# Kernel tuning notes

Measured on AMD Instinct MI355X. Metric: run time of the kernel, lower is better.

The kernel has to match this reference:

```python
import jax, jax.numpy as jnp
import numpy as np

N = 50000
E = 800000
R = 8
F_IN = 128
H = 128          # num_hidden
F_OUT = 128      # num_outputs
D1, D2, D3 = 2 * H, H, F_OUT


def _glorot(key, shape):
    fan_in, fan_out = shape[-2], shape[-1]
    lim = np.sqrt(6.0 / (fan_in + fan_out)).astype(np.float32)
    return jax.random.uniform(key, shape, jnp.float32, -lim, lim)


def setup_inputs() -> dict:
    key = jax.random.key(0)
    ks = jax.random.split(key, 12)
    x = jax.random.normal(ks[0], (N, F_IN), jnp.float32)
    edge_index = jax.random.randint(ks[1], (2, E), 0, N, jnp.int64)
    edge_type = jax.random.randint(ks[2], (E,), 0, R, jnp.int64)
    return {
        "x": x,
        "edge_index": edge_index,
        "edge_type": edge_type,
        "w1": _glorot(ks[3], (R, F_IN, D1)),
        "root1": _glorot(ks[4], (F_IN, D1)),
        "b1": jnp.zeros((D1,), jnp.float32),
        "w2": _glorot(ks[5], (R, D1, D2)),
        "root2": _glorot(ks[6], (D1, D2)),
        "b2": jnp.zeros((D2,), jnp.float32),
        "w3": _glorot(ks[7], (R, D2, D3)),
        "root3": _glorot(ks[8], (D2, D3)),
        "b3": jnp.zeros((D3,), jnp.float32),
    }


def _rgcn_layer(h, src, dst, seg, inv_cnt, W, root, bias):
    # Per-relation mean aggregation via a fused (dst, rel) segment id,
    # then a grouped contraction with the per-relation weights.
    n, fin = h.shape
    s = jax.ops.segment_sum(h[src], seg, num_segments=n * R)  # [N*R, fin]
    agg = s.reshape(n, R, fin) * inv_cnt                      # mean per (node, rel)
    return jnp.einsum("nri,rio->no", agg, W) + h @ root + bias


def reference(x, edge_index, edge_type, w1, root1, b1, w2, root2, b2, w3, root3, b3):
    src, dst = edge_index[0], edge_index[1]
    seg = dst * R + edge_type                                  # fused (dst, rel) id
    cnt = jax.ops.segment_sum(jnp.ones((E,), x.dtype), seg, num_segments=N * R)
    inv_cnt = (1.0 / jnp.maximum(cnt, 1.0)).reshape(N, R, 1)

    h1 = jax.nn.elu(_rgcn_layer(x, src, dst, seg, inv_cnt, w1, root1, b1))
    # dropout: identity (eval mode)
    h2 = jax.nn.elu(_rgcn_layer(h1, src, dst, seg, inv_cnt, w2, root2, b2))
    h3 = jax.nn.elu(_rgcn_layer(h2, src, dst, seg, inv_cnt, w3, root3, b3))
    return jnp.concatenate([h1, h2, h3], axis=1)               # [N, D1+D2+D3]
```

## Files before the change

### kernel.cpp

```cpp
#include <hip/hip_runtime.h>


#define DEVI __device__ __forceinline__

constexpr int NN    = 50000;
constexpr int EE    = 800000;
constexpr int RREL  = 8;
constexpr int NRSEG = NN * RREL;

using u16 = unsigned short;
using u32 = unsigned int;
using u64 = unsigned long long;

typedef short short8 __attribute__((ext_vector_type(8)));
typedef float f32x4  __attribute__((ext_vector_type(4)));

DEVI float bf2f(u32 u){ union{u32 i; float f;} x; x.i = u << 16; return x.f; }
DEVI u16   f2b(float f){ u32 u = __float_as_uint(f); u32 r = u + 0x7fffu + ((u >> 16) & 1u); return (u16)(r >> 16); }

typedef const __attribute__((address_space(1))) u32 gas_u32;
typedef __attribute__((address_space(3))) u32       las_u32;
DEVI void gload16(const void* g, void* l){
  __builtin_amdgcn_global_load_lds((gas_u32*)(u64)g, (las_u32*)(u64)l, 16, 0, 0);
}


__global__ void count_k(const int* __restrict__ dst, const int* __restrict__ et, int* __restrict__ cnt){
  int e = blockIdx.x * 256 + threadIdx.x;
  if(e < EE) atomicAdd(&cnt[dst[e] * RREL + et[e]], 1);
}

constexpr int SCAN_E = 8;
constexpr int CHUNK  = 2048;
constexpr int NB     = (NRSEG + CHUNK - 1) / CHUNK;

__global__ void scan1_k(const int* __restrict__ cnt, int* __restrict__ bsums){
  __shared__ int sm[256];
  int b = blockIdx.x, t = threadIdx.x;
  int base = b * CHUNK + t * SCAN_E;
  int s = 0;
  #pragma unroll
  for(int j = 0; j < SCAN_E; j++){ int i = base + j; s += (i < NRSEG) ? cnt[i] : 0; }
  sm[t] = s; __syncthreads();
  for(int off = 128; off > 0; off >>= 1){ if(t < off) sm[t] += sm[t + off]; __syncthreads(); }
  if(t == 0) bsums[b] = sm[0];
}

__global__ void scan2_k(int* __restrict__ bsums){
  __shared__ int sm[256];
  int t = threadIdx.x;
  int v = (t < NB) ? bsums[t] : 0;
  sm[t] = v; __syncthreads();
  for(int off = 1; off < 256; off <<= 1){
    int x = (t >= off) ? sm[t - off] : 0; __syncthreads();
    sm[t] += x; __syncthreads();
  }
  if(t < NB) bsums[t] = sm[t] - v;
}

__global__ void scan3_k(const int* __restrict__ cnt, const int* __restrict__ bsums, int* __restrict__ offs){
  __shared__ int sm[256];
  int b = blockIdx.x, t = threadIdx.x;
  int base = b * CHUNK + t * SCAN_E;
  int loc[SCAN_E]; int run = 0;
  #pragma unroll
  for(int j = 0; j < SCAN_E; j++){ int i = base + j; int c = (i < NRSEG) ? cnt[i] : 0; loc[j] = run; run += c; }
  sm[t] = run; __syncthreads();
  for(int off = 1; off < 256; off <<= 1){
    int x = (t >= off) ? sm[t - off] : 0; __syncthreads();
    sm[t] += x; __syncthreads();
  }
  int tb = bsums[b] + sm[t] - run;
  #pragma unroll
  for(int j = 0; j < SCAN_E; j++){ int i = base + j; if(i < NRSEG) offs[i] = tb + loc[j]; }
  if(b == 0 && t == 0) offs[NRSEG] = EE;
}

__global__ void fill_k(const int* __restrict__ src, const int* __restrict__ dst, const int* __restrict__ et,
                       const int* __restrict__ offs, int* __restrict__ fill, int* __restrict__ ssrc){
  int e = blockIdx.x * 256 + threadIdx.x;
  if(e < EE){
    int seg = dst[e] * RREL + et[e];
    int r = atomicAdd(&fill[seg], 1);
    ssrc[offs[seg] + r] = src[e];
  }
}

__global__ void inv_k(const int* __restrict__ cnt, float* __restrict__ inv){
  int i = blockIdx.x * 256 + threadIdx.x;
  if(i < NRSEG){ int c = cnt[i]; inv[i] = 1.0f / (float)(c > 0 ? c : 1); }
}

__global__ void castx_k(const float* __restrict__ x, u16* __restrict__ xb){
  int i = blockIdx.x * 256 + threadIdx.x;
  if(i < NN * 128) xb[i] = f2b(x[i]);
}

__global__ void packw_k(const float* __restrict__ w, const float* __restrict__ root,
                        u16* __restrict__ wp, int FIN, int FOUT){
  int idx = blockIdx.x * 256 + threadIdx.x;
  int tot = (RREL + 1) * FIN * FOUT;
  if(idx < tot){
    int i = idx % FIN;
    int o = (idx / FIN) % FOUT;
    int g = idx / (FIN * FOUT);
    float v = (g < RREL) ? w[((size_t)g * FIN + i) * FOUT + o] : root[(size_t)i * FOUT + o];
    wp[idx] = f2b(v);
  }
}


DEVI void acc8(float* a, uint4 v){
  a[0] += bf2f(v.x & 0xffffu); a[1] += bf2f(v.x >> 16);
  a[2] += bf2f(v.y & 0xffffu); a[3] += bf2f(v.y >> 16);
  a[4] += bf2f(v.z & 0xffffu); a[5] += bf2f(v.z >> 16);
  a[6] += bf2f(v.w & 0xffffu); a[7] += bf2f(v.w >> 16);
}

template<int FIN, int RSUB>
__global__ __launch_bounds__(256)
void agg_k(const u16* __restrict__ hb, const int* __restrict__ ssrc,
           const int* __restrict__ offs, const float* __restrict__ inv,
           u16* __restrict__ agg, int r0)
{
  constexpr int G   = FIN / 8;
  constexpr int LDW = RSUB * FIN;
  const int gl  = threadIdx.x & (G - 1);
  int gid = (int)((blockIdx.x * blockDim.x + threadIdx.x) / G);
  const int ng = (int)((gridDim.x * blockDim.x) / G);
  const int S = NN * RSUB;
  for(int s = gid; s < S; s += ng){
    int n = s / RSUB, rr = s - n * RSUB;
    int seg = n * RREL + r0 + rr;
    int beg = offs[seg], end = offs[seg + 1];
    float sc = inv[seg];
    float acc[8];
    #pragma unroll
    for(int i = 0; i < 8; i++) acc[i] = 0.f;
    int e = beg;
    for(; e + 2 <= end; e += 2){
      int s0 = ssrc[e], s1 = ssrc[e + 1];
      uint4 v0 = ((const uint4*)(hb + (size_t)s0 * FIN))[gl];
      uint4 v1 = ((const uint4*)(hb + (size_t)s1 * FIN))[gl];
      acc8(acc, v0);
      acc8(acc, v1);
    }
    if(e < end){
      uint4 v0 = ((const uint4*)(hb + (size_t)ssrc[e] * FIN))[gl];
      acc8(acc, v0);
    }
    uint4 o;
    o.x = (u32)f2b(acc[0] * sc) | ((u32)f2b(acc[1] * sc) << 16);
    o.y = (u32)f2b(acc[2] * sc) | ((u32)f2b(acc[3] * sc) << 16);
    o.z = (u32)f2b(acc[4] * sc) | ((u32)f2b(acc[5] * sc) << 16);
    o.w = (u32)f2b(acc[6] * sc) | ((u32)f2b(acc[7] * sc) << 16);
    ((uint4*)(agg + (size_t)n * LDW + rr * FIN))[gl] = o;
  }
}


template<int FIN, int NAGG, bool ROOT, int FOUT>
__global__ __launch_bounds__(512)
void gemm_k(const u16* __restrict__ Aagg, const u16* __restrict__ Aroot,
            const u16* __restrict__ Wagg, const u16* __restrict__ Wroot,
            const float* __restrict__ bias, float* __restrict__ dout,
            u16* __restrict__ hbout)
{
  static_assert(FIN % 32 == 0, "");
  constexpr int KSG = FIN / 32;
  constexpr int NG  = NAGG + (ROOT ? 1 : 0);
  constexpr int NKS = NG * KSG;
  constexpr int LDA = NAGG * FIN;
  constexpr int WN    = (FOUT == 256) ? 4 : 2;
  constexpr int WM    = 8 / WN;
  constexpr int WROWS = 128 / WM;
  constexpr int MREP  = WROWS / 16;
  constexpr int ASL = 512;
  constexpr int BSL = FOUT * 4;
  constexpr int LPS = 1 + BSL / 512;
  __shared__ u16 lds[3][(ASL + BSL) * 8];
  const int bm  = (int)blockIdx.x;
  const int tid = threadIdx.x;
  const int wid = tid >> 6, lane = tid & 63;
  const int wm  = wid / WN, wn = wid % WN;

  auto stage = [&](int ks, u16* l){
    u16* lA = l;
    u16* lB = l + ASL * 8;
    int g    = ks / KSG;
    int koff = (ks - g * KSG) * 32;
    bool isRoot = ROOT && (g == NAGG);
    {
      int sb = wid * 64;
      int s  = sb + lane;
      int pair = s >> 3, cs = s & 7;
      int c    = cs ^ (pair & 7);
      int row  = pair * 2 + (c >> 2);
      int k8   = c & 3;
      int kk   = koff + k8 * 8;
      int rowg = bm * 128 + row; rowg = rowg < NN ? rowg : NN - 1;
      const u16* ga = isRoot ? (Aroot + (size_t)rowg * FIN + kk)
                             : (Aagg + (size_t)rowg * LDA + g * FIN + kk);
      gload16(ga, lA + sb * 8);
    }
    #pragma unroll
    for(int rnd = 0; rnd < BSL / 512; rnd++){
      int sb = rnd * 512 + wid * 64;
      int s  = sb + lane;
      int pair = s >> 3, cs = s & 7;
      int c    = cs ^ (pair & 7);
      int row  = pair * 2 + (c >> 2);
      int k8   = c & 3;
      int kk   = koff + k8 * 8;
      const u16* gb = isRoot ? (Wroot + (size_t)row * FIN + kk)
                             : (Wagg + ((size_t)g * FOUT + row) * FIN + kk);
      gload16(gb, lB + sb * 8);
    }
  };

  auto ldfrag = [&](const u16* buf, int row, int k8){
    int pair = row >> 1;
    int c    = ((row & 1) << 2) + k8;
    int cs   = c ^ (pair & 7);
    return *(const short8*)(buf + pair * 64 + cs * 8);
  };

  f32x4 acc[MREP][4] = {};

  stage(0, (u16*)lds[0]);
  stage(1, (u16*)lds[1]);
  for(int ks = 0; ks < NKS; ks++){
    if(ks + 1 < NKS){
      asm volatile("s_waitcnt vmcnt(%0)" :: "i"(LPS) : "memory");
    } else {
      asm volatile("s_waitcnt vmcnt(0)" ::: "memory");
    }
    __builtin_amdgcn_sched_barrier(0);
    __builtin_amdgcn_s_barrier();
    __builtin_amdgcn_sched_barrier(0);
    if(ks + 2 < NKS) stage(ks + 2, (u16*)lds[(ks + 2) % 3]);
    const u16* lA = (const u16*)lds[ks % 3];
    const u16* lB = lA + ASL * 8;
    short8 af[MREP], bf4[4];
    #pragma unroll
    for(int m = 0; m < MREP; m++) af[m] = ldfrag(lA, wm * WROWS + m * 16 + (lane & 15), lane >> 4);
    #pragma unroll
    for(int n = 0; n < 4; n++) bf4[n] = ldfrag(lB, wn * 64 + n * 16 + (lane & 15), lane >> 4);
    #pragma unroll
    for(int m = 0; m < MREP; m++)
      #pragma unroll
      for(int n = 0; n < 4; n++)
        acc[m][n] = __builtin_amdgcn_mfma_f32_16x16x32_bf16(af[m], bf4[n], acc[m][n], 0, 0, 0);
  }

  #pragma unroll
  for(int m = 0; m < MREP; m++){
    #pragma unroll
    for(int j = 0; j < 4; j++){
      int grow = bm * 128 + wm * WROWS + m * 16 + (lane >> 4) * 4 + j;
      if(grow >= NN) continue;
      #pragma unroll
      for(int n = 0; n < 4; n++){
        int gcol = wn * 64 + n * 16 + (lane & 15);
        float v = acc[m][n][j];
        v += bias[gcol];
        v = v > 0.f ? v : expm1f(v);
        dout[(size_t)grow * 512 + gcol] = v;
        if(hbout) hbout[(size_t)grow * FOUT + gcol] = f2b(v);
      }
    }
  }
}


extern "C" void kernel_launch(void* const* d_in, const int* in_sizes, int n_in,
                              void* d_out, int out_size, void* d_ws, size_t ws_size,
                              hipStream_t stream)
{
  const float* x     = (const float*)d_in[0];
  const int*   ei    = (const int*)d_in[1];
  const int*   et    = (const int*)d_in[2];
  const float* w1    = (const float*)d_in[3];
  const float* root1 = (const float*)d_in[4];
  const float* b1    = (const float*)d_in[5];
  const float* w2    = (const float*)d_in[6];
  const float* root2 = (const float*)d_in[7];
  const float* b2    = (const float*)d_in[8];
  const float* w3    = (const float*)d_in[9];
  const float* root3 = (const float*)d_in[10];
  const float* b3    = (const float*)d_in[11];
  float* out = (float*)d_out;

  const int* esrc = ei;
  const int* edst = ei + EE;

  char* w = (char*)d_ws;
  auto alloc = [&](size_t bytes)->char*{ char* p = w; w += (bytes + 255) & ~(size_t)255; return p; };
  int*   cnt   = (int*)  alloc((size_t)NRSEG * 4);
  int*   offs  = (int*)  alloc((size_t)(NRSEG + 1) * 4);
  int*   fill  = (int*)  alloc((size_t)NRSEG * 4);
  float* inv   = (float*)alloc((size_t)NRSEG * 4);
  int*   ssrc  = (int*)  alloc((size_t)EE * 4);
  u16*   xb    = (u16*)  alloc((size_t)NN * 128 * 2);
  u16*   h1b   = (u16*)  alloc((size_t)NN * 256 * 2);
  u16*   h2b   = (u16*)  alloc((size_t)NN * 128 * 2);
  u16*   wp1   = (u16*)  alloc((size_t)9 * 256 * 128 * 2);
  u16*   wp2   = (u16*)  alloc((size_t)9 * 256 * 128 * 2);
  u16*   wp3   = (u16*)  alloc((size_t)9 * 128 * 128 * 2);
  int*   bsums = (int*)  alloc(1024 * 4);
  u16*   agg   = (u16*)  alloc((size_t)NN * 2048 * 2);
  (void)ws_size; (void)in_sizes; (void)n_in; (void)out_size;

  hipMemsetAsync(cnt,  0, (size_t)NRSEG * 4, stream);
  hipMemsetAsync(fill, 0, (size_t)NRSEG * 4, stream);

  count_k<<<(EE + 255) / 256, 256, 0, stream>>>(edst, et, cnt);
  scan1_k<<<NB, 256, 0, stream>>>(cnt, bsums);
  scan2_k<<<1, 256, 0, stream>>>(bsums);
  scan3_k<<<NB, 256, 0, stream>>>(cnt, bsums, offs);
  fill_k<<<(EE + 255) / 256, 256, 0, stream>>>(esrc, edst, et, offs, fill, ssrc);
  inv_k<<<(NRSEG + 255) / 256, 256, 0, stream>>>(cnt, inv);
  castx_k<<<(NN * 128 + 255) / 256, 256, 0, stream>>>(x, xb);

  packw_k<<<(9 * 128 * 256 + 255) / 256, 256, 0, stream>>>(w1, root1, wp1, 128, 256);
  packw_k<<<(9 * 256 * 128 + 255) / 256, 256, 0, stream>>>(w2, root2, wp2, 256, 128);
  packw_k<<<(9 * 128 * 128 + 255) / 256, 256, 0, stream>>>(w3, root3, wp3, 128, 128);

  const int MT = (NN + 127) / 128;

  agg_k<128, 8><<<4096, 256, 0, stream>>>(xb, ssrc, offs, inv, agg, 0);
  gemm_k<128, 8, true, 256><<<MT, 512, 0, stream>>>(
      agg, xb, wp1, wp1 + (size_t)8 * 256 * 128, b1, out + 0, h1b);

  agg_k<256, 8><<<4096, 256, 0, stream>>>(h1b, ssrc, offs, inv, agg, 0);
  gemm_k<256, 8, true, 128><<<MT, 512, 0, stream>>>(
      agg, h1b, wp2, wp2 + (size_t)8 * 128 * 256, b2, out + 256, h2b);

  agg_k<128, 8><<<4096, 256, 0, stream>>>(h2b, ssrc, offs, inv, agg, 0);
  gemm_k<128, 8, true, 128><<<MT, 512, 0, stream>>>(
      agg, h2b, wp3, wp3 + (size_t)8 * 128 * 128, b3, out + 384, nullptr);
}
```

Measured before the change: 476.3 us.

## Transform-then-aggregate for layers 2 and 3 to gather narrower features

For layers 2 and 3, node features are first multiplied by all 8 relation weights plus the root weight in a new dense GEMM, producing a per-node bf16 table of width 1152. A scatter kernel then gathers the per-relation 128-wide slices from that table per edge, applies the mean scaling, adds the root term and bias, and applies ELU. This reorders the computation so layer 2 gathers 128-wide rows instead of 256-wide ones and no longer writes or reads the large per-(node,relation) aggregate buffer. The cost is a sizable intermediate table write/read and an extra rounding of transformed features to bf16.

```diff
diff --git a/kernel.cpp b/kernel.cpp
--- a/kernel.cpp
+++ b/kernel.cpp
@@ -7,6 +7,7 @@
 constexpr int EE    = 800000;
 constexpr int RREL  = 8;
 constexpr int NRSEG = NN * RREL;
+constexpr int NTC   = 1152;
 
 using u16 = unsigned short;
 using u32 = unsigned int;
@@ -273,6 +274,161 @@
 }
 
 
+template<int FIN>
+__global__ __launch_bounds__(512)
+void dgemm_k(const u16* __restrict__ A, const u16* __restrict__ Bw, u16* __restrict__ T)
+{
+  constexpr int NKS = FIN / 32;
+  constexpr int ASL = 512;
+  constexpr int BSL = 512;
+  constexpr int LPS = 2;
+  __shared__ u16 lds[3][(ASL + BSL) * 8];
+  const int bid = (int)blockIdx.x;
+  const int bm  = bid / 9;
+  const int jc  = bid % 9;
+  const int tid = threadIdx.x;
+  const int wid = tid >> 6, lane = tid & 63;
+  const int wm  = wid >> 1, wn = wid & 1;
+
+  auto stage = [&](int ks, u16* l){
+    u16* lA = l;
+    u16* lB = l + ASL * 8;
+    int koff = ks * 32;
+    {
+      int sb = wid * 64;
+      int s  = sb + lane;
+      int pair = s >> 3, cs = s & 7;
+      int c    = cs ^ (pair & 7);
+      int row  = pair * 2 + (c >> 2);
+      int k8   = c & 3;
+      int kk   = koff + k8 * 8;
+      int rowg = bm * 128 + row; rowg = rowg < NN ? rowg : NN - 1;
+      gload16(A + (size_t)rowg * FIN + kk, lA + sb * 8);
+    }
+    {
+      int sb = wid * 64;
+      int s  = sb + lane;
+      int pair = s >> 3, cs = s & 7;
+      int c    = cs ^ (pair & 7);
+      int row  = pair * 2 + (c >> 2);
+      int k8   = c & 3;
+      int kk   = koff + k8 * 8;
+      gload16(Bw + ((size_t)(jc * 128 + row)) * FIN + kk, lB + sb * 8);
+    }
+  };
+
+  auto ldfrag = [&](const u16* buf, int row, int k8){
+    int pair = row >> 1;
+    int c    = ((row & 1) << 2) + k8;
+    int cs   = c ^ (pair & 7);
+    return *(const short8*)(buf + pair * 64 + cs * 8);
+  };
+
+  f32x4 acc[2][4] = {};
+
+  stage(0, (u16*)lds[0]);
+  stage(1, (u16*)lds[1]);
+  for(int ks = 0; ks < NKS; ks++){
+    if(ks + 1 < NKS){
+      asm volatile("s_waitcnt vmcnt(%0)" :: "i"(LPS) : "memory");
+    } else {
+      asm volatile("s_waitcnt vmcnt(0)" ::: "memory");
+    }
+    __builtin_amdgcn_sched_barrier(0);
+    __builtin_amdgcn_s_barrier();
+    __builtin_amdgcn_sched_barrier(0);
+    if(ks + 2 < NKS) stage(ks + 2, (u16*)lds[(ks + 2) % 3]);
+    const u16* lA = (const u16*)lds[ks % 3];
+    const u16* lB = lA + ASL * 8;
+    short8 af[2], bf4[4];
+    #pragma unroll
+    for(int m = 0; m < 2; m++) af[m] = ldfrag(lA, wm * 32 + m * 16 + (lane & 15), lane >> 4);
+    #pragma unroll
+    for(int n = 0; n < 4; n++) bf4[n] = ldfrag(lB, wn * 64 + n * 16 + (lane & 15), lane >> 4);
+    #pragma unroll
+    for(int m = 0; m < 2; m++)
+      #pragma unroll
+      for(int n = 0; n < 4; n++)
+        acc[m][n] = __builtin_amdgcn_mfma_f32_16x16x32_bf16(af[m], bf4[n], acc[m][n], 0, 0, 0);
+  }
+
+  #pragma unroll
+  for(int m = 0; m < 2; m++){
+    #pragma unroll
+    for(int j = 0; j < 4; j++){
+      int grow = bm * 128 + wm * 32 + m * 16 + (lane >> 4) * 4 + j;
+      if(grow >= NN) continue;
+      #pragma unroll
+      for(int n = 0; n < 4; n++){
+        int gcol = wn * 64 + n * 16 + (lane & 15);
+        T[(size_t)grow * NTC + jc * 128 + gcol] = f2b(acc[m][n][j]);
+      }
+    }
+  }
+}
+
+
+template<bool HB>
+__global__ __launch_bounds__(256)
+void scat_k(const u16* __restrict__ T, const int* __restrict__ ssrc,
+            const int* __restrict__ offs, const float* __restrict__ inv,
+            const float* __restrict__ bias, float* __restrict__ dout, int dcol0,
+            u16* __restrict__ hbout)
+{
+  const int gl = threadIdx.x & 15;
+  int n = (int)((blockIdx.x * 256 + threadIdx.x) >> 4);
+  if(n >= NN) return;
+  float acc[8];
+  #pragma unroll
+  for(int i = 0; i < 8; i++) acc[i] = 0.f;
+  {
+    uint4 v = *(const uint4*)(T + (size_t)n * NTC + 1024 + gl * 8);
+    acc8(acc, v);
+  }
+  const int base = n * RREL;
+  int e = offs[base];
+  for(int r = 0; r < RREL; r++){
+    int eend = offs[base + r + 1];
+    int col = r * 128 + gl * 8;
+    float tmp[8];
+    #pragma unroll
+    for(int i = 0; i < 8; i++) tmp[i] = 0.f;
+    for(; e + 2 <= eend; e += 2){
+      int s0 = ssrc[e], s1 = ssrc[e + 1];
+      uint4 v0 = *(const uint4*)(T + (size_t)s0 * NTC + col);
+      uint4 v1 = *(const uint4*)(T + (size_t)s1 * NTC + col);
+      acc8(tmp, v0);
+      acc8(tmp, v1);
+    }
+    if(e < eend){
+      uint4 v0 = *(const uint4*)(T + (size_t)ssrc[e] * NTC + col);
+      acc8(tmp, v0);
+      e++;
+    }
+    float sc = inv[base + r];
+    #pragma unroll
+    for(int i = 0; i < 8; i++) acc[i] += sc * tmp[i];
+  }
+  float o[8];
+  #pragma unroll
+  for(int i = 0; i < 8; i++){
+    float v = acc[i] + bias[gl * 8 + i];
+    o[i] = v > 0.f ? v : expm1f(v);
+  }
+  float4* dp = (float4*)(dout + (size_t)n * 512 + dcol0 + gl * 8);
+  dp[0] = make_float4(o[0], o[1], o[2], o[3]);
+  dp[1] = make_float4(o[4], o[5], o[6], o[7]);
+  if(HB){
+    uint4 hv;
+    hv.x = (u32)f2b(o[0]) | ((u32)f2b(o[1]) << 16);
+    hv.y = (u32)f2b(o[2]) | ((u32)f2b(o[3]) << 16);
+    hv.z = (u32)f2b(o[4]) | ((u32)f2b(o[5]) << 16);
+    hv.w = (u32)f2b(o[6]) | ((u32)f2b(o[7]) << 16);
+    *(uint4*)(hbout + (size_t)n * 128 + gl * 8) = hv;
+  }
+}
+
+
 extern "C" void kernel_launch(void* const* d_in, const int* in_sizes, int n_in,
                               void* d_out, int out_size, void* d_ws, size_t ws_size,
                               hipStream_t stream)
@@ -308,7 +464,8 @@
   u16*   wp2   = (u16*)  alloc((size_t)9 * 256 * 128 * 2);
   u16*   wp3   = (u16*)  alloc((size_t)9 * 128 * 128 * 2);
   int*   bsums = (int*)  alloc(1024 * 4);
-  u16*   agg   = (u16*)  alloc((size_t)NN * 2048 * 2);
+  u16*   agg   = (u16*)  alloc((size_t)NN * 1024 * 2);
+  u16*   T     = (u16*)  alloc((size_t)NN * NTC * 2);
   (void)ws_size; (void)in_sizes; (void)n_in; (void)out_size;
 
   hipMemsetAsync(cnt,  0, (size_t)NRSEG * 4, stream);
@@ -327,16 +484,15 @@
   packw_k<<<(9 * 128 * 128 + 255) / 256, 256, 0, stream>>>(w3, root3, wp3, 128, 128);
 
   const int MT = (NN + 127) / 128;
+  const int SB = (NN * 16 + 255) / 256;
 
   agg_k<128, 8><<<4096, 256, 0, stream>>>(xb, ssrc, offs, inv, agg, 0);
   gemm_k<128, 8, true, 256><<<MT, 512, 0, stream>>>(
       agg, xb, wp1, wp1 + (size_t)8 * 256 * 128, b1, out + 0, h1b);
 
-  agg_k<256, 8><<<4096, 256, 0, stream>>>(h1b, ssrc, offs, inv, agg, 0);
-  gemm_k<256, 8, true, 128><<<MT, 512, 0, stream>>>(
-      agg, h1b, wp2, wp2 + (size_t)8 * 128 * 256, b2, out + 256, h2b);
-
-  agg_k<128, 8><<<4096, 256, 0, stream>>>(h2b, ssrc, offs, inv, agg, 0);
-  gemm_k<128, 8, true, 128><<<MT, 512, 0, stream>>>(
-      agg, h2b, wp3, wp3 + (size_t)8 * 128 * 128, b3, out + 384, nullptr);
-}
+  dgemm_k<256><<<MT * 9, 512, 0, stream>>>(h1b, wp2, T);
+  scat_k<true><<<SB, 256, 0, stream>>>(T, ssrc, offs, inv, b2, out, 256, h2b);
+
+  dgemm_k<128><<<MT * 9, 512, 0, stream>>>(h2b, wp3, T);
+  scat_k<false><<<SB, 256, 0, stream>>>(T, ssrc, offs, inv, b3, out, 384, nullptr);
+}
```

Result: faster. 438.1 us (-8.0%).
